# Kernel optimization log

Measured on AMD Instinct MI355X. Metric: run time of the kernel, lower is better.

The kernel has to match this reference:

```python
import jax, jax.numpy as jnp
import numpy as np

N, C_IN, C_OUT = 8192, 128, 128
BN_EPS = 1e-5
EDGE_PROB = 0.004  # avg degree ~33


def setup_inputs() -> dict:
    key = jax.random.key(0)
    k1, k2, k3, k4, k5, k6 = jax.random.split(key, 6)
    node_features = jax.random.normal(k1, (N, C_IN), dtype=jnp.float32)
    # binary dense adjacency (rand fill, thresholded to ~avg degree 33)
    adjacency_matrix = (jax.random.uniform(k2, (N, N)) < EDGE_PROB).astype(jnp.float32)
    s = 1.0 / np.sqrt(C_IN)
    W_n = jax.random.uniform(k3, (C_OUT, C_IN), jnp.float32, -s, s)
    b_n = jax.random.uniform(k4, (C_OUT,), jnp.float32, -s, s)
    W_c = jax.random.uniform(k5, (C_OUT, C_IN), jnp.float32, -s, s)
    b_c = jax.random.uniform(k6, (C_OUT,), jnp.float32, -s, s)
    gamma = jnp.ones((C_OUT,), jnp.float32)
    beta = jnp.zeros((C_OUT,), jnp.float32)
    return {"node_features": node_features, "adjacency_matrix": adjacency_matrix,
            "W_n": W_n, "b_n": b_n, "W_c": W_c, "b_c": b_c,
            "gamma": gamma, "beta": beta}


def reference(node_features, adjacency_matrix, W_n, b_n, W_c, b_c, gamma, beta):
    # mean aggregation: degrees from row-sums (as in the torch code), agg = A.T @ X / deg
    deg = adjacency_matrix.sum(axis=1, keepdims=True)          # [N,1]
    deg = jnp.where(deg == 0, jnp.ones_like(deg), deg)
    agg = (adjacency_matrix.T @ node_features) / deg           # [N,C_in]
    h = agg @ W_n.T + b_n + node_features @ W_c.T + b_c        # [N,C_out]
    # BatchNorm1d, training-mode batch stats (biased variance)
    mu = h.mean(axis=0)
    var = ((h - mu) ** 2).mean(axis=0)
    h_norm = (h - mu) * jax.lax.rsqrt(var + BN_EPS)
    return jax.nn.relu(gamma * h_norm + beta)
```

## Files before the change

kernel.cpp:

```cpp
#include <hip/hip_runtime.h>
#include <stdint.h>

#define NN 8192
#define CC 128
#define BN_EPS 1e-5f

__device__ inline unsigned short f2bf(float f) {
    unsigned int u = __float_as_uint(f);
    unsigned int r = (u + 0x7fffu + ((u >> 16) & 1u)) >> 16;
    return (unsigned short)r;
}
__device__ inline float bf2f(unsigned short s) {
    return __uint_as_float(((unsigned int)s) << 16);
}

__global__ __launch_bounds__(256) void k1a_mask(
        const float* __restrict__ A, unsigned long long* __restrict__ Mt,
        float* __restrict__ deg) {
    const int lane = threadIdx.x & 63;
    const int task = blockIdx.x * 4 + (threadIdx.x >> 6);
    const int band = task >> 5;
    const int i0   = (task & 31) << 8;
    const int j0   = band << 6;

    const float4* Ap = reinterpret_cast<const float4*>(A + (size_t)j0 * NN + i0) + lane;
    unsigned long long m0 = 0, m1 = 0, m2 = 0, m3 = 0;
    int degc = 0;

    #pragma unroll 8
    for (int j = 0; j < 64; ++j) {
        float4 v = Ap[(size_t)j * (NN / 4)];
        bool n0 = v.x != 0.0f, n1 = v.y != 0.0f, n2 = v.z != 0.0f, n3 = v.w != 0.0f;
        unsigned long long b0 = __ballot(n0), b1 = __ballot(n1);
        unsigned long long b2 = __ballot(n2), b3 = __ballot(n3);
        const unsigned long long bit = 1ull << j;
        if (n0) m0 |= bit;
        if (n1) m1 |= bit;
        if (n2) m2 |= bit;
        if (n3) m3 |= bit;
        int cnt = __popcll(b0) + __popcll(b1) + __popcll(b2) + __popcll(b3);
        if (lane == j) degc = cnt;
    }

    atomicAdd(&deg[j0 + lane], (float)degc);
    unsigned long long* p = Mt + (size_t)band * NN + i0 + 4 * lane;
    reinterpret_cast<ulonglong2*>(p)[0] = make_ulonglong2(m0, m1);
    reinterpret_cast<ulonglong2*>(p)[1] = make_ulonglong2(m2, m3);
}

__global__ __launch_bounds__(256) void k1c_gather(
        const unsigned long long* __restrict__ Mt, const float* __restrict__ X,
        const float* __restrict__ deg, float* __restrict__ aggN) {
    const int lane = threadIdx.x & 63;
    const int i = blockIdx.x * 4 + (threadIdx.x >> 6);

    unsigned long long w0 = Mt[(size_t)(2 * lane) * NN + i];
    unsigned long long w1 = Mt[(size_t)(2 * lane + 1) * NN + i];
    float acc0 = 0.0f, acc1 = 0.0f;

    unsigned long long any = __ballot((w0 | w1) != 0ull);
    while (any) {
        int q = __builtin_ctzll(any); any &= any - 1;
        unsigned long long u0 = __shfl(w0, q);
        unsigned long long u1 = __shfl(w1, q);
        const float* Xq = X + (size_t)q * 128 * CC;
        while (u0) {
            int b = __builtin_ctzll(u0); u0 &= u0 - 1;
            const float* xr = Xq + b * CC;
            acc0 += xr[lane];
            acc1 += xr[64 + lane];
        }
        while (u1) {
            int b = __builtin_ctzll(u1); u1 &= u1 - 1;
            const float* xr = Xq + (b + 64) * CC;
            acc0 += xr[lane];
            acc1 += xr[64 + lane];
        }
    }

    float d  = deg[i];
    float rd = (d == 0.0f) ? 1.0f : (1.0f / d);
    aggN[(size_t)i * CC + lane]      = acc0 * rd;
    aggN[(size_t)i * CC + 64 + lane] = acc1 * rd;
}

__global__ __launch_bounds__(256, 2) void k2_gemm(
        const float* __restrict__ aggN, const float* __restrict__ X,
        const float* __restrict__ Wn, const float* __restrict__ bn,
        const float* __restrict__ Wc, const float* __restrict__ bc,
        float* __restrict__ h, float* __restrict__ bsum, float* __restrict__ bsq) {
    __shared__ unsigned short WtN[128 * 128];
    __shared__ unsigned short WtC[128 * 128];
    const int tid = threadIdx.x;
    for (int idx = tid * 4; idx < 128 * 128; idx += 1024) {
        float4 wn4 = *reinterpret_cast<const float4*>(Wn + idx);
        float4 wc4 = *reinterpret_cast<const float4*>(Wc + idx);
        int c = idx >> 7, k0 = idx & 127;
        WtN[(k0 + 0) * 128 + c] = f2bf(wn4.x);
        WtN[(k0 + 1) * 128 + c] = f2bf(wn4.y);
        WtN[(k0 + 2) * 128 + c] = f2bf(wn4.z);
        WtN[(k0 + 3) * 128 + c] = f2bf(wn4.w);
        WtC[(k0 + 0) * 128 + c] = f2bf(wc4.x);
        WtC[(k0 + 1) * 128 + c] = f2bf(wc4.y);
        WtC[(k0 + 2) * 128 + c] = f2bf(wc4.z);
        WtC[(k0 + 3) * 128 + c] = f2bf(wc4.w);
    }
    __syncthreads();
    const int c  = tid & 127;
    const int rg = tid >> 7;
    const int i0 = blockIdx.x * 16 + rg * 8;

    float accN[8], accC[8];
    #pragma unroll
    for (int r = 0; r < 8; ++r) { accN[r] = 0.0f; accC[r] = 0.0f; }

    float4 ar[8], xr[8], an[8], xn[8];

#define LOADK(ab_, xb_, k_) do {                                               \
    _Pragma("unroll")                                                          \
    for (int r = 0; r < 8; ++r) {                                              \
        ab_[r] = *reinterpret_cast<const float4*>(&aggN[(size_t)(i0 + r) * CC + (k_)]); \
        xb_[r] = *reinterpret_cast<const float4*>(&X[(size_t)(i0 + r) * CC + (k_)]);    \
    }                                                                          \
} while (0)

#define COMPK(ab_, xb_, k_) do {                                               \
    _Pragma("unroll")                                                          \
    for (int kk = 0; kk < 4; ++kk) {                                           \
        float wn_ = bf2f(WtN[((k_) + kk) * 128 + c]);                          \
        float wc_ = bf2f(WtC[((k_) + kk) * 128 + c]);                          \
        _Pragma("unroll")                                                      \
        for (int r = 0; r < 8; ++r) {                                          \
            accN[r] = fmaf((&ab_[r].x)[kk], wn_, accN[r]);                     \
            accC[r] = fmaf((&xb_[r].x)[kk], wc_, accC[r]);                     \
        }                                                                      \
    }                                                                          \
} while (0)

    LOADK(ar, xr, 0);
    for (int k = 0; k < 128; k += 8) {
        LOADK(an, xn, k + 4);
        COMPK(ar, xr, k);
        if (k + 8 < 128) LOADK(ar, xr, k + 8);
        COMPK(an, xn, k + 4);
    }

    const float bnc = bn[c], bcc = bc[c];
    float sp = 0.0f, sq = 0.0f;
    #pragma unroll
    for (int r = 0; r < 8; ++r) {
        float hv = accN[r] + accC[r] + bnc + bcc;
        h[(size_t)(i0 + r) * CC + c] = hv;
        sp += hv; sq += hv * hv;
    }
    __syncthreads();
    float* red = reinterpret_cast<float*>(WtN);
    red[rg * 128 + c]       = sp;
    red[256 + rg * 128 + c] = sq;
    __syncthreads();
    if (rg == 0) {
        atomicAdd(&bsum[c], red[c] + red[128 + c]);
        atomicAdd(&bsq[c],  red[256 + c] + red[384 + c]);
    }
}

__global__ __launch_bounds__(256) void k4_bn(
        const float* __restrict__ h, const float* __restrict__ bsum,
        const float* __restrict__ bsq, const float* __restrict__ gamma,
        const float* __restrict__ beta, float* __restrict__ out) {
    const int idx = (blockIdx.x * 256 + threadIdx.x) * 4;
    const int c0  = idx & 127;
    float4 hv = *reinterpret_cast<const float4*>(h + idx);
    float4 s4 = *reinterpret_cast<const float4*>(bsum + c0);
    float4 q4 = *reinterpret_cast<const float4*>(bsq + c0);
    float4 g4 = *reinterpret_cast<const float4*>(gamma + c0);
    float4 b4 = *reinterpret_cast<const float4*>(beta + c0);
    const float invN = 1.0f / 8192.0f;
    float4 o;
    const float* hp = &hv.x; const float* sp = &s4.x; const float* qp = &q4.x;
    const float* gp = &g4.x; const float* bp = &b4.x; float* op = &o.x;
    #pragma unroll
    for (int jj = 0; jj < 4; ++jj) {
        float mu  = sp[jj] * invN;
        float var = qp[jj] * invN - mu * mu;
        float sc  = gp[jj] * rsqrtf(var + BN_EPS);
        float v   = (hp[jj] - mu) * sc + bp[jj];
        op[jj] = v > 0.0f ? v : 0.0f;
    }
    *reinterpret_cast<float4*>(out + idx) = o;
}

extern "C" void kernel_launch(void* const* d_in, const int* in_sizes, int n_in,
                              void* d_out, int out_size, void* d_ws, size_t ws_size,
                              hipStream_t stream) {
    const float* X     = (const float*)d_in[0];
    const float* A     = (const float*)d_in[1];
    const float* Wn    = (const float*)d_in[2];
    const float* bn    = (const float*)d_in[3];
    const float* Wc    = (const float*)d_in[4];
    const float* bc    = (const float*)d_in[5];
    const float* gamma = (const float*)d_in[6];
    const float* beta  = (const float*)d_in[7];
    float* out = (float*)d_out;

    char* ws = (char*)d_ws;
    float* deg  = (float*)(ws);
    float* bsum = (float*)(ws + 32768);
    float* bsq  = (float*)(ws + 33280);
    float* aggN = (float*)(ws + 65536);
    unsigned long long* Mt = (unsigned long long*)(ws + 4259840);
    float* h    = (float*)(ws + 4259840);

    hipMemsetAsync(d_ws, 0, 33792, stream);

    k1a_mask  <<<1024, 256, 0, stream>>>(A, Mt, deg);
    k1c_gather<<<2048, 256, 0, stream>>>(Mt, X, deg, aggN);
    k2_gemm   <<<512,  256, 0, stream>>>(aggN, X, Wn, bn, Wc, bc, h, bsum, bsq);
    k4_bn     <<<1024, 256, 0, stream>>>(h, bsum, bsq, gamma, beta, out);
}
```

Before: 464.7 us.

## Split mask and gather work finer across waves with shared-memory reductions

```diff
diff --git a/kernel.cpp b/kernel.cpp
--- a/kernel.cpp
+++ b/kernel.cpp
@@ -14,74 +14,80 @@
     return __uint_as_float(((unsigned int)s) << 16);
 }
 
-__global__ __launch_bounds__(256) void k1a_mask(
+__global__ __launch_bounds__(256, 8) void k1a_mask(
         const float* __restrict__ A, unsigned long long* __restrict__ Mt,
         float* __restrict__ deg) {
+    __shared__ float dred[4][64];
     const int lane = threadIdx.x & 63;
-    const int task = blockIdx.x * 4 + (threadIdx.x >> 6);
-    const int band = task >> 5;
-    const int i0   = (task & 31) << 8;
+    const int wave = threadIdx.x >> 6;
+    const int task = blockIdx.x * 4 + wave;
+    const int band = task >> 6;
+    const int i0   = (task & 63) << 7;
     const int j0   = band << 6;
 
-    const float4* Ap = reinterpret_cast<const float4*>(A + (size_t)j0 * NN + i0) + lane;
-    unsigned long long m0 = 0, m1 = 0, m2 = 0, m3 = 0;
-    int degc = 0;
+    const uint2* Ap = reinterpret_cast<const uint2*>(A + (size_t)j0 * NN + i0) + lane;
+    unsigned long long m0 = 0, m1 = 0;
+    float degc = 0.0f;
 
     #pragma unroll 8
     for (int j = 0; j < 64; ++j) {
-        float4 v = Ap[(size_t)j * (NN / 4)];
-        bool n0 = v.x != 0.0f, n1 = v.y != 0.0f, n2 = v.z != 0.0f, n3 = v.w != 0.0f;
+        uint2 v = Ap[(size_t)j * (NN / 2)];
+        bool n0 = v.x != 0u, n1 = v.y != 0u;
         unsigned long long b0 = __ballot(n0), b1 = __ballot(n1);
-        unsigned long long b2 = __ballot(n2), b3 = __ballot(n3);
         const unsigned long long bit = 1ull << j;
         if (n0) m0 |= bit;
         if (n1) m1 |= bit;
-        if (n2) m2 |= bit;
-        if (n3) m3 |= bit;
-        int cnt = __popcll(b0) + __popcll(b1) + __popcll(b2) + __popcll(b3);
-        if (lane == j) degc = cnt;
-    }
-
-    atomicAdd(&deg[j0 + lane], (float)degc);
-    unsigned long long* p = Mt + (size_t)band * NN + i0 + 4 * lane;
-    reinterpret_cast<ulonglong2*>(p)[0] = make_ulonglong2(m0, m1);
-    reinterpret_cast<ulonglong2*>(p)[1] = make_ulonglong2(m2, m3);
-}
-
-__global__ __launch_bounds__(256) void k1c_gather(
+        if (lane == j) degc = (float)(__popcll(b0) + __popcll(b1));
+    }
+
+    unsigned long long* p = Mt + (size_t)band * NN + i0 + 2 * lane;
+    *reinterpret_cast<ulonglong2*>(p) = make_ulonglong2(m0, m1);
+
+    dred[wave][lane] = degc;
+    __syncthreads();
+    if (wave == 0) {
+        float s = dred[0][lane] + dred[1][lane] + dred[2][lane] + dred[3][lane];
+        atomicAdd(&deg[j0 + lane], s);
+    }
+}
+
+__global__ __launch_bounds__(256, 8) void k1c_gather(
         const unsigned long long* __restrict__ Mt, const float* __restrict__ X,
         const float* __restrict__ deg, float* __restrict__ aggN) {
+    __shared__ float red[4][128];
     const int lane = threadIdx.x & 63;
-    const int i = blockIdx.x * 4 + (threadIdx.x >> 6);
-
-    unsigned long long w0 = Mt[(size_t)(2 * lane) * NN + i];
-    unsigned long long w1 = Mt[(size_t)(2 * lane + 1) * NN + i];
+    const int wave = threadIdx.x >> 6;
+    const int i = blockIdx.x;
+
+    unsigned long long w = 0;
+    if (lane < 32)
+        w = Mt[(size_t)(wave * 32 + lane) * NN + i];
     float acc0 = 0.0f, acc1 = 0.0f;
 
-    unsigned long long any = __ballot((w0 | w1) != 0ull);
+    unsigned long long any = __ballot(w != 0ull);
     while (any) {
         int q = __builtin_ctzll(any); any &= any - 1;
-        unsigned long long u0 = __shfl(w0, q);
-        unsigned long long u1 = __shfl(w1, q);
-        const float* Xq = X + (size_t)q * 128 * CC;
-        while (u0) {
-            int b = __builtin_ctzll(u0); u0 &= u0 - 1;
+        unsigned long long u = __shfl(w, q);
+        const float* Xq = X + (size_t)((wave * 32 + q) * 64) * CC;
+        while (u) {
+            int b = __builtin_ctzll(u); u &= u - 1;
             const float* xr = Xq + b * CC;
             acc0 += xr[lane];
             acc1 += xr[64 + lane];
         }
-        while (u1) {
-            int b = __builtin_ctzll(u1); u1 &= u1 - 1;
-            const float* xr = Xq + (b + 64) * CC;
-            acc0 += xr[lane];
-            acc1 += xr[64 + lane];
-        }
-    }
-
-    float d  = deg[i];
-    float rd = (d == 0.0f) ? 1.0f : (1.0f / d);
-    aggN[(size_t)i * CC + lane]      = acc0 * rd;
-    aggN[(size_t)i * CC + 64 + lane] = acc1 * rd;
+    }
+
+    red[wave][lane]      = acc0;
+    red[wave][64 + lane] = acc1;
+    __syncthreads();
+    if (wave == 0) {
+        float s0 = red[0][lane]      + red[1][lane]      + red[2][lane]      + red[3][lane];
+        float s1 = red[0][64 + lane] + red[1][64 + lane] + red[2][64 + lane] + red[3][64 + lane];
+        float d  = deg[i];
+        float rd = (d == 0.0f) ? 1.0f : (1.0f / d);
+        aggN[(size_t)i * CC + lane]      = s0 * rd;
+        aggN[(size_t)i * CC + 64 + lane] = s1 * rd;
+    }
 }
 
 __global__ __launch_bounds__(256, 2) void k2_gemm(
@@ -213,8 +219,8 @@
 
     hipMemsetAsync(d_ws, 0, 33792, stream);
 
-    k1a_mask  <<<1024, 256, 0, stream>>>(A, Mt, deg);
-    k1c_gather<<<2048, 256, 0, stream>>>(Mt, X, deg, aggN);
+    k1a_mask  <<<2048, 256, 0, stream>>>(A, Mt, deg);
+    k1c_gather<<<8192, 256, 0, stream>>>(Mt, X, deg, aggN);
     k2_gemm   <<<512,  256, 0, stream>>>(aggN, X, Wn, bn, Wc, bc, h, bsum, bsq);
     k4_bn     <<<1024, 256, 0, stream>>>(h, bsum, bsq, gamma, beta, out);
 }
```

Result: no change. 459.7 us (-1.1%).
